# Performance work log

Measured on AMD Instinct MI355X. Metric: run time of the kernel, lower is better.

The kernel has to match this reference:

```python
import jax, jax.numpy as jnp
import numpy as np

B, N, K = 2, 16384, 8
NH, HD, CH, KV_IN = 4, 32, 128, 128
EPS = 1e-5

def layer_norm(x, g, b):
    mu = x.mean(-1, keepdims=True)
    var = ((x - mu) ** 2).mean(-1, keepdims=True)
    return (x - mu) / jnp.sqrt(var + EPS) * g + b

def setup_inputs() -> dict:
    key = jax.random.key(0)
    ks = jax.random.split(key, 8)
    s = 0.02
    return {
        "query_in": jax.random.normal(ks[0], (B, N, CH), jnp.float32),
        "kv_in": jax.random.normal(ks[1], (B, N, K, KV_IN), jnp.float32),
        "w_kv": jax.random.normal(ks[2], (KV_IN, 2 * NH * HD), jnp.float32) * s,
        "w_q": jax.random.normal(ks[3], (CH, NH * HD), jnp.float32) * s,
        "w_mh": jax.random.normal(ks[4], (NH * HD, CH), jnp.float32) * s,
        "b_mh": jnp.zeros((CH,), jnp.float32),
        "w1": jax.random.normal(ks[5], (CH, CH), jnp.float32) * s,
        "b1": jnp.zeros((CH,), jnp.float32),
        "w2": jax.random.normal(ks[6], (CH, CH), jnp.float32) * s,
        "b2": jnp.zeros((CH,), jnp.float32),
        "ln1_g": jnp.ones((CH,), jnp.float32),
        "ln1_b": jnp.zeros((CH,), jnp.float32),
        "ln2_g": jnp.ones((CH,), jnp.float32),
        "ln2_b": jnp.zeros((CH,), jnp.float32),
    }

def reference(query_in, kv_in, w_kv, w_q, w_mh, b_mh, w1, b1, w2, b2,
              ln1_g, ln1_b, ln2_g, ln2_b):
    # q projection: [B,N,CH] -> [B,N,NH,HD]
    q = (query_in @ w_q).reshape(B, N, NH, HD)
    # kv projection: [B,N,K,KV_IN] -> [B,N,K,2,NH,HD]; chunk(2) on last dim
    kv = (kv_in @ w_kv).reshape(B, N, K, 2, NH, HD)
    k, v = kv[..., 0, :, :], kv[..., 1, :, :]  # each [B,N,K,NH,HD]
    # per-token local attention over its own K keys
    sim = jnp.einsum('bnhd,bnkhd->bnhk', q, k) / np.sqrt(HD).astype(np.float32)
    attn = jax.nn.softmax(sim, axis=-1)
    out = jnp.einsum('bnhk,bnkhd->bnhd', attn, v).reshape(B, N, NH * HD)
    out = out @ w_mh + b_mh
    res = layer_norm(out, ln1_g, ln1_b) + query_in
    # GELU MLP (torch nn.GELU default = exact erf form)
    mlp = jax.nn.gelu(res @ w1 + b1, approximate=False) @ w2 + b2
    return layer_norm(mlp + res, ln2_g, ln2_b)
```

## Files before the change

### kernel.cpp

```cpp
#include <hip/hip_runtime.h>
#include <hip/hip_fp16.h>

typedef _Float16 f16x8 __attribute__((ext_vector_type(8)));
typedef float f32x4 __attribute__((ext_vector_type(4)));
typedef unsigned int uint32;

#define LDW 136
#define TB  16

#define WAITLGKM() do { __builtin_amdgcn_s_waitcnt(0xC07F); __builtin_amdgcn_sched_barrier(0); } while(0)

union F16x8U { f16x8 v; __half2 h2[4]; uint2 u2[2]; };

__device__ __forceinline__ uint32 pk2f(float a, float b) {
  __half2 h = __floats2half2_rn(a, b);
  return *reinterpret_cast<uint32*>(&h);
}
__device__ __forceinline__ float bcast(float v, int sl) {
  return __int_as_float(__builtin_amdgcn_readlane(__float_as_int(v), sl));
}
__device__ __forceinline__ float wred_sum(float v) {
  v += __shfl_xor(v, 32); v += __shfl_xor(v, 16); v += __shfl_xor(v, 8);
  v += __shfl_xor(v, 4);  v += __shfl_xor(v, 2);  v += __shfl_xor(v, 1);
  return v;
}
__device__ __forceinline__ f16x8 ldsv8(const __half* p) {
  return *reinterpret_cast<const f16x8*>(p);
}
__device__ __forceinline__ f32x4 mfma16(f16x8 a, f16x8 b, f32x4 c) {
  return __builtin_amdgcn_mfma_f32_16x16x32_f16(a, b, c, 0, 0, 0);
}
__device__ __forceinline__ void stp(__half* base, int fr, int fq, int nt, f32x4 a) {
  uint2 u; u.x = pk2f(a[0], a[1]); u.y = pk2f(a[2], a[3]);
  *reinterpret_cast<uint2*>(&base[fr * LDW + nt * 16 + fq * 4]) = u;
}

#define OFF_WQ   0
#define OFF_WK2  16384
#define OFF_WV   36864
#define OFF_WMH  53248
#define OFF_W1   69632
#define OFF_W2   86016
#define WS_HALVES 102400

__global__ void prep_weights(const float* __restrict__ wq, const float* __restrict__ wkv,
                             const float* __restrict__ wmh, const float* __restrict__ w1,
                             const float* __restrict__ w2, __half* __restrict__ ws) {
  int idx = blockIdx.x * 256 + threadIdx.x;
  if (idx >= WS_HALVES) return;
  float v;
  if (idx < OFF_WK2) {
    int t = idx, c = t >> 7, k = t & 127;
    v = wq[k * 128 + c];
  } else if (idx < OFF_WV) {
    int t = idx - OFF_WK2;
    int d = t % 40, row = t / 40;
    int h = row >> 7, i = row & 127;
    v = (d < 32) ? wkv[i * 256 + h * 32 + d] : 0.f;
  } else if (idx < OFF_WMH) {
    int t = idx - OFF_WV, c = t >> 7, k = t & 127;
    v = wkv[k * 256 + 128 + c];
  } else if (idx < OFF_W1) {
    int t = idx - OFF_WMH, c = t >> 7, k = t & 127;
    v = wmh[k * 128 + c];
  } else if (idx < OFF_W2) {
    int t = idx - OFF_W1, c = t >> 7, k = t & 127;
    v = w1[k * 128 + c];
  } else {
    int t = idx - OFF_W2, c = t >> 7, k = t & 127;
    v = w2[k * 128 + c];
  }
  ws[idx] = __float2half_rn(v);
}

#define LOADB2(GOFF, NT0, NT1, BF) do {                                          \
  _Pragma("unroll")                                                              \
  for (int t_ = 0; t_ < 2; ++t_) {                                               \
    int nt_ = t_ ? (NT1) : (NT0);                                                \
    _Pragma("unroll")                                                            \
    for (int ks_ = 0; ks_ < 4; ++ks_)                                            \
      BF[t_][ks_] = *reinterpret_cast<const f16x8*>(                             \
          wsv + (GOFF) + (nt_*16 + fr)*128 + ks_*32 + fq*8);                     \
  } } while (0)

#define GEMM2(AT, BF, ACC0, ACC1) do {                                           \
  _Pragma("unroll")                                                              \
  for (int ks_ = 0; ks_ < 4; ++ks_) {                                            \
    f16x8 b_ = ldsv8(&(AT)[fr * LDW + ks_ * 32 + fq * 8]);                       \
    ACC0 = mfma16(BF[0][ks_], b_, ACC0);                                         \
    ACC1 = mfma16(BF[1][ks_], b_, ACC1);                                         \
  } } while (0)

__global__ void __launch_bounds__(256, 6) ca_mfma(
    const float* __restrict__ xq, const float* __restrict__ kvin,
    const __half* __restrict__ wsv,
    const float* __restrict__ bmh, const float* __restrict__ b1,
    const float* __restrict__ b2,
    const float* __restrict__ g1, const float* __restrict__ bb1,
    const float* __restrict__ g2, const float* __restrict__ bb2,
    float* __restrict__ outp)
{
  __shared__ __half QWC[64 * LDW];
  __shared__ __half UBUF[2 * TB * LDW];

  const int tid = threadIdx.x;
  const int wv = tid >> 6, lane = tid & 63;
  const int fr = lane & 15, fq = lane >> 4;
  const int tb = blockIdx.x * TB;
  const int ltb = wv * 4;

  __half* Xh = UBUF;
  __half* Qb = UBUF + 2176;
  __half* Ob = UBUF;
  __half* Yb   = QWC;
  __half* RESb = QWC + 16 * LDW;
  __half* Hb   = QWC + 32 * LDW;
  __half* Vb   = QWC + 48 * LDW;

  const f32x4 ZZ = {0.f, 0.f, 0.f, 0.f};

  float4 pre[4];
  {
    const float4* kv4 = reinterpret_cast<const float4*>(kvin + (size_t)(tb + ltb) * 1024);
    pre[0] = kv4[2 * lane];       pre[1] = kv4[2 * lane + 1];
    pre[2] = kv4[2 * lane + 128]; pre[3] = kv4[2 * lane + 129];
  }
  f16x8 bf[2][4];
  LOADB2(OFF_WQ, wv, 4 + wv, bf);

  {
    int tok = tid >> 4, ko = (tid & 15) * 8;
    const float4* s0 = reinterpret_cast<const float4*>(xq + (size_t)(tb + tok) * 128 + ko);
    float4 a = s0[0], b = s0[1];
    uint4 u; u.x = pk2f(a.x, a.y); u.y = pk2f(a.z, a.w);
    u.z = pk2f(b.x, b.y); u.w = pk2f(b.z, b.w);
    *reinterpret_cast<uint4*>(&Xh[tok * LDW + ko]) = u;
  }
  __syncthreads();

  {
    f32x4 aA = ZZ, aB = ZZ;
    GEMM2(Xh, bf, aA, aB);
    stp(Qb, fr, fq, wv, aA);
    stp(Qb, fr, fq, 4 + wv, aB);
  }
  f16x8 bq[8];
#pragma unroll
  for (int nt = 0; nt < 8; ++nt)
    bq[nt] = *reinterpret_cast<const f16x8*>(
        wsv + OFF_WK2 + (wv * 128 + nt * 16 + fr) * 40 + fq * 8);
  __syncthreads();

  {
    f16x8 aq = ldsv8(&Qb[fr * LDW + wv * 32 + fq * 8]);
#pragma unroll
    for (int nt = 0; nt < 8; ++nt) {
      f32x4 acc = mfma16(bq[nt], aq, ZZ);
      uint2 u; u.x = pk2f(acc[0], acc[1]); u.y = pk2f(acc[2], acc[3]);
      *reinterpret_cast<uint2*>(&QWC[(wv * 16 + fr) * LDW + nt * 16 + fq * 4]) = u;
    }
  }
  __syncthreads();

  {
    const int p = lane & 31, hh = p >> 3, kk = p & 7, hf = lane >> 5;
    const int kr = lane >> 4, i8 = (lane & 15) * 8;
    const int l2 = 2 * lane;
    __half* kvw = UBUF + wv * 1088;
#pragma unroll 1
    for (int lt = 0; lt < 4; ++lt) {
      const int ltok = ltb + lt;
      WAITLGKM();
      {
        uint4 u0, u1;
        u0.x = pk2f(pre[0].x, pre[0].y); u0.y = pk2f(pre[0].z, pre[0].w);
        u0.z = pk2f(pre[1].x, pre[1].y); u0.w = pk2f(pre[1].z, pre[1].w);
        u1.x = pk2f(pre[2].x, pre[2].y); u1.y = pk2f(pre[2].z, pre[2].w);
        u1.z = pk2f(pre[3].x, pre[3].y); u1.w = pk2f(pre[3].z, pre[3].w);
        *reinterpret_cast<uint4*>(&kvw[kr * LDW + i8]) = u0;
        *reinterpret_cast<uint4*>(&kvw[(4 + kr) * LDW + i8]) = u1;
      }
      if (lt < 3) {
        const float4* kv4 = reinterpret_cast<const float4*>(kvin + (size_t)(tb + ltok + 1) * 1024);
        pre[0] = kv4[2 * lane];       pre[1] = kv4[2 * lane + 1];
        pre[2] = kv4[2 * lane + 128]; pre[3] = kv4[2 * lane + 129];
      }
      WAITLGKM();
      const __half* qrow = &QWC[(hh * 16 + ltok) * LDW + hf * 64];
      const __half* krow = &kvw[kk * LDW + hf * 64];
      __half2 s0 = __floats2half2_rn(0.f, 0.f), s1 = s0;
#pragma unroll
      for (int e = 0; e < 8; ++e) {
        F16x8U q8, k8;
        q8.v = ldsv8(qrow + e * 8);
        k8.v = ldsv8(krow + e * 8);
        s0 = __hfma2(q8.h2[0], k8.h2[0], s0);
        s1 = __hfma2(q8.h2[1], k8.h2[1], s1);
        s0 = __hfma2(q8.h2[2], k8.h2[2], s0);
        s1 = __hfma2(q8.h2[3], k8.h2[3], s1);
      }
      s0 = __hadd2(s0, s1);
      float acc = (__low2float(s0) + __high2float(s0)) * 0.17677669529663687f;
      acc += __shfl_xor(acc, 32);
      float m = acc;
      m = fmaxf(m, __shfl_xor(m, 1));
      m = fmaxf(m, __shfl_xor(m, 2));
      m = fmaxf(m, __shfl_xor(m, 4));
      float e = __expf(acc - m);
      float sden = e;
      sden += __shfl_xor(sden, 1); sden += __shfl_xor(sden, 2); sden += __shfl_xor(sden, 4);
      float at = __fdividef(e, sden);
      __half2 kvc[8];
#pragma unroll
      for (int k = 0; k < 8; ++k)
        kvc[k] = *reinterpret_cast<const __half2*>(&kvw[k * LDW + l2]);
#pragma unroll
      for (int h = 0; h < 4; ++h) {
        float c0 = 0.f, c1 = 0.f;
#pragma unroll
        for (int k = 0; k < 8; ++k) {
          float a = bcast(at, h * 8 + k);
          float2 kf = __half22float2(kvc[k]);
          c0 = fmaf(a, kf.x, c0);
          c1 = fmaf(a, kf.y, c1);
        }
        *reinterpret_cast<__half2*>(&QWC[(h * 16 + ltok) * LDW + l2]) =
            __floats2half2_rn(c0, c1);
      }
    }
  }
  LOADB2(OFF_WV, wv, 4 + wv, bf);
  __syncthreads();

  float2 xr[4];
#pragma unroll
  for (int lt = 0; lt < 4; ++lt) {
    int tok = tb + ltb + lt;
    xr[lt] = *reinterpret_cast<const float2*>(&xq[(size_t)tok * 128 + 2 * lane]);
  }
  {
    const int h1 = wv >> 1, h2 = 2 + (wv >> 1);
    f32x4 a1c = ZZ, a2c = ZZ;
#pragma unroll
    for (int ks = 0; ks < 4; ++ks) {
      f16x8 b1f = ldsv8(&QWC[(h1 * 16 + fr) * LDW + ks * 32 + fq * 8]);
      a1c = mfma16(bf[0][ks], b1f, a1c);
      f16x8 b2f = ldsv8(&QWC[(h2 * 16 + fr) * LDW + ks * 32 + fq * 8]);
      a2c = mfma16(bf[1][ks], b2f, a2c);
    }
    stp(Ob, fr, fq, wv, a1c);
    stp(Ob, fr, fq, 4 + wv, a2c);
  }
  LOADB2(OFF_WMH, wv, 4 + wv, bf);
  __syncthreads();

  {
    f32x4 aA = ZZ, aB = ZZ;
    GEMM2(Ob, bf, aA, aB);
    stp(Yb, fr, fq, wv, aA);
    stp(Yb, fr, fq, 4 + wv, aB);
  }
  LOADB2(OFF_W1, wv, 4 + wv, bf);
  __syncthreads();

  {
    const int l2 = 2 * lane;
    float2 bm = *reinterpret_cast<const float2*>(&bmh[l2]);
    float2 gg = *reinterpret_cast<const float2*>(&g1[l2]);
    float2 cc = *reinterpret_cast<const float2*>(&bb1[l2]);
#pragma unroll
    for (int lt = 0; lt < 4; ++lt) {
      int row = ltb + lt;
      float2 y = __half22float2(*reinterpret_cast<const __half2*>(&Yb[row * LDW + l2]));
      float v0 = y.x + bm.x, v1 = y.y + bm.y;
      float s = wred_sum(v0 + v1);
      float sq = wred_sum(v0 * v0 + v1 * v1);
      float mu = s * 0.0078125f;
      float var = sq * 0.0078125f - mu * mu;
      float rstd = rsqrtf(var + 1e-5f);
      float r0 = (v0 - mu) * rstd * gg.x + cc.x + xr[lt].x;
      float r1 = (v1 - mu) * rstd * gg.y + cc.y + xr[lt].y;
      *reinterpret_cast<__half2*>(&RESb[row * LDW + l2]) = __floats2half2_rn(r0, r1);
    }
  }
  __syncthreads();

  {
    f32x4 aA = ZZ, aB = ZZ;
    GEMM2(RESb, bf, aA, aB);
    int c0 = wv * 16 + fq * 4, c1 = 64 + wv * 16 + fq * 4;
    float4 b1a = *reinterpret_cast<const float4*>(&b1[c0]);
    float4 b1b = *reinterpret_cast<const float4*>(&b1[c1]);
    uint2 ua, ub;
    float t0, t1;
    t0 = aA[0] + b1a.x; t0 = 0.5f * t0 * (1.f + erff(t0 * 0.70710678118654752f));
    t1 = aA[1] + b1a.y; t1 = 0.5f * t1 * (1.f + erff(t1 * 0.70710678118654752f));
    ua.x = pk2f(t0, t1);
    t0 = aA[2] + b1a.z; t0 = 0.5f * t0 * (1.f + erff(t0 * 0.70710678118654752f));
    t1 = aA[3] + b1a.w; t1 = 0.5f * t1 * (1.f + erff(t1 * 0.70710678118654752f));
    ua.y = pk2f(t0, t1);
    t0 = aB[0] + b1b.x; t0 = 0.5f * t0 * (1.f + erff(t0 * 0.70710678118654752f));
    t1 = aB[1] + b1b.y; t1 = 0.5f * t1 * (1.f + erff(t1 * 0.70710678118654752f));
    ub.x = pk2f(t0, t1);
    t0 = aB[2] + b1b.z; t0 = 0.5f * t0 * (1.f + erff(t0 * 0.70710678118654752f));
    t1 = aB[3] + b1b.w; t1 = 0.5f * t1 * (1.f + erff(t1 * 0.70710678118654752f));
    ub.y = pk2f(t0, t1);
    *reinterpret_cast<uint2*>(&Hb[fr * LDW + c0]) = ua;
    *reinterpret_cast<uint2*>(&Hb[fr * LDW + c1]) = ub;
  }
  LOADB2(OFF_W2, wv, 4 + wv, bf);
  __syncthreads();

  {
    f32x4 aA = ZZ, aB = ZZ;
    GEMM2(Hb, bf, aA, aB);
    int c0 = wv * 16 + fq * 4, c1 = 64 + wv * 16 + fq * 4;
    float4 b2a = *reinterpret_cast<const float4*>(&b2[c0]);
    float4 b2b = *reinterpret_cast<const float4*>(&b2[c1]);
    F16x8U ra, rb;
    ra.u2[0] = *reinterpret_cast<const uint2*>(&RESb[fr * LDW + c0]);
    rb.u2[0] = *reinterpret_cast<const uint2*>(&RESb[fr * LDW + c1]);
    uint2 ua, ub;
    float2 p0 = __half22float2(ra.h2[0]), p1 = __half22float2(ra.h2[1]);
    ua.x = pk2f(aA[0] + b2a.x + p0.x, aA[1] + b2a.y + p0.y);
    ua.y = pk2f(aA[2] + b2a.z + p1.x, aA[3] + b2a.w + p1.y);
    float2 p2 = __half22float2(rb.h2[0]), p3 = __half22float2(rb.h2[1]);
    ub.x = pk2f(aB[0] + b2b.x + p2.x, aB[1] + b2b.y + p2.y);
    ub.y = pk2f(aB[2] + b2b.z + p3.x, aB[3] + b2b.w + p3.y);
    *reinterpret_cast<uint2*>(&Vb[fr * LDW + c0]) = ua;
    *reinterpret_cast<uint2*>(&Vb[fr * LDW + c1]) = ub;
  }
  __syncthreads();

  {
    const int l2 = 2 * lane;
    float2 gg = *reinterpret_cast<const float2*>(&g2[l2]);
    float2 cc = *reinterpret_cast<const float2*>(&bb2[l2]);
#pragma unroll
    for (int lt = 0; lt < 4; ++lt) {
      int row = ltb + lt, tok = tb + row;
      float2 v = __half22float2(*reinterpret_cast<const __half2*>(&Vb[row * LDW + l2]));
      float s = wred_sum(v.x + v.y);
      float sq = wred_sum(v.x * v.x + v.y * v.y);
      float mu = s * 0.0078125f;
      float var = sq * 0.0078125f - mu * mu;
      float rstd = rsqrtf(var + 1e-5f);
      float2 o;
      o.x = (v.x - mu) * rstd * gg.x + cc.x;
      o.y = (v.y - mu) * rstd * gg.y + cc.y;
      *reinterpret_cast<float2*>(&outp[(size_t)tok * 128 + l2]) = o;
    }
  }
}

extern "C" void kernel_launch(void* const* d_in, const int* in_sizes, int n_in,
                              void* d_out, int out_size, void* d_ws, size_t ws_size,
                              hipStream_t stream) {
  const float* xq = (const float*)d_in[0];
  const float* kv = (const float*)d_in[1];
  const float* wkv = (const float*)d_in[2];
  const float* wq = (const float*)d_in[3];
  const float* wmh = (const float*)d_in[4];
  const float* bmh = (const float*)d_in[5];
  const float* w1 = (const float*)d_in[6];
  const float* b1 = (const float*)d_in[7];
  const float* w2 = (const float*)d_in[8];
  const float* b2 = (const float*)d_in[9];
  const float* g1 = (const float*)d_in[10];
  const float* bb1 = (const float*)d_in[11];
  const float* g2 = (const float*)d_in[12];
  const float* bb2 = (const float*)d_in[13];
  __half* ws = (__half*)d_ws;

  prep_weights<<<(WS_HALVES + 255) / 256, 256, 0, stream>>>(wq, wkv, wmh, w1, w2, ws);

  const int tokens = 32768;
  ca_mfma<<<tokens / TB, 256, 0, stream>>>(xq, kv, ws, bmh, b1, b2,
                                           g1, bb1, g2, bb2, (float*)d_out);
}
```

Before: 65.62 us.

## Double token tile to 32 with 512-thread blocks and shuffle-based Q transpose

Doubles the tokens per block to 32 and the block size to 512 threads (8 waves split into two 16-token halves). Each wave's weight fragments now cover more tokens, and there are fewer blocks in total. The Q projection result is rearranged into the MFMA operand layout with cross-lane shuffles instead of a round trip through LDS, which removes one barrier. The trade-offs are a larger LDS footprint per block and a 512-thread launch bound that may lower occupancy.

```diff
diff --git a/kernel.cpp b/kernel.cpp
--- a/kernel.cpp
+++ b/kernel.cpp
@@ -6,11 +6,11 @@
 typedef unsigned int uint32;
 
 #define LDW 136
-#define TB  16
+#define TB  32
 
 #define WAITLGKM() do { __builtin_amdgcn_s_waitcnt(0xC07F); __builtin_amdgcn_sched_barrier(0); } while(0)
 
-union F16x8U { f16x8 v; __half2 h2[4]; uint2 u2[2]; };
+union F16x8U { f16x8 v; __half2 h2[4]; uint2 u2[2]; uint4 u4; };
 
 __device__ __forceinline__ uint32 pk2f(float a, float b) {
   __half2 h = __floats2half2_rn(a, b);
@@ -91,7 +91,7 @@
     ACC1 = mfma16(BF[1][ks_], b_, ACC1);                                         \
   } } while (0)
 
-__global__ void __launch_bounds__(256, 6) ca_mfma(
+__global__ void __launch_bounds__(512, 6) ca_mfma(
     const float* __restrict__ xq, const float* __restrict__ kvin,
     const __half* __restrict__ wsv,
     const float* __restrict__ bmh, const float* __restrict__ b1,
@@ -100,22 +100,22 @@
     const float* __restrict__ g2, const float* __restrict__ bb2,
     float* __restrict__ outp)
 {
-  __shared__ __half QWC[64 * LDW];
-  __shared__ __half UBUF[2 * TB * LDW];
+  __shared__ __half QWC[128 * LDW];
+  __shared__ __half UBUF[8 * 1088];
 
   const int tid = threadIdx.x;
   const int wv = tid >> 6, lane = tid & 63;
+  const int wl = wv & 3, tt = wv >> 2;
   const int fr = lane & 15, fq = lane >> 4;
   const int tb = blockIdx.x * TB;
   const int ltb = wv * 4;
 
   __half* Xh = UBUF;
-  __half* Qb = UBUF + 2176;
   __half* Ob = UBUF;
   __half* Yb   = QWC;
-  __half* RESb = QWC + 16 * LDW;
-  __half* Hb   = QWC + 32 * LDW;
-  __half* Vb   = QWC + 48 * LDW;
+  __half* RESb = QWC + 32 * LDW;
+  __half* Hb   = QWC + 64 * LDW;
+  __half* Vb   = QWC + 96 * LDW;
 
   const f32x4 ZZ = {0.f, 0.f, 0.f, 0.f};
 
@@ -126,7 +126,7 @@
     pre[2] = kv4[2 * lane + 128]; pre[3] = kv4[2 * lane + 129];
   }
   f16x8 bf[2][4];
-  LOADB2(OFF_WQ, wv, 4 + wv, bf);
+  LOADB2(OFF_WQ, 2 * wl, 2 * wl + 1, bf);
 
   {
     int tok = tid >> 4, ko = (tid & 15) * 8;
@@ -138,26 +138,37 @@
   }
   __syncthreads();
 
+  f16x8 aq;
   {
     f32x4 aA = ZZ, aB = ZZ;
-    GEMM2(Xh, bf, aA, aB);
-    stp(Qb, fr, fq, wv, aA);
-    stp(Qb, fr, fq, 4 + wv, aB);
-  }
-  f16x8 bq[8];
-#pragma unroll
-  for (int nt = 0; nt < 8; ++nt)
-    bq[nt] = *reinterpret_cast<const f16x8*>(
-        wsv + OFF_WK2 + (wv * 128 + nt * 16 + fr) * 40 + fq * 8);
-  __syncthreads();
-
-  {
-    f16x8 aq = ldsv8(&Qb[fr * LDW + wv * 32 + fq * 8]);
+    GEMM2(Xh + tt * 16 * LDW, bf, aA, aB);
+    uint32 w0a = pk2f(aA[0], aA[1]), w1a = pk2f(aA[2], aA[3]);
+    uint32 w0b = pk2f(aB[0], aB[1]), w1b = pk2f(aB[2], aB[3]);
+    int srcA = fr + 32 * (fq & 1), srcB = srcA + 16;
+    uint32 a0A = (uint32)__shfl((int)w0a, srcA), a1A = (uint32)__shfl((int)w1a, srcA);
+    uint32 b0A = (uint32)__shfl((int)w0b, srcA), b1A = (uint32)__shfl((int)w1b, srcA);
+    uint32 a0B = (uint32)__shfl((int)w0a, srcB), a1B = (uint32)__shfl((int)w1a, srcB);
+    uint32 b0B = (uint32)__shfl((int)w0b, srcB), b1B = (uint32)__shfl((int)w1b, srcB);
+    bool thi = (fq >> 1) != 0;
+    F16x8U bu;
+    bu.u4.x = thi ? b0A : a0A;
+    bu.u4.y = thi ? b1A : a1A;
+    bu.u4.z = thi ? b0B : a0B;
+    bu.u4.w = thi ? b1B : a1B;
+    aq = bu.v;
+  }
+
+  {
+    f16x8 bq[8];
+#pragma unroll
+    for (int nt = 0; nt < 8; ++nt)
+      bq[nt] = *reinterpret_cast<const f16x8*>(
+          wsv + OFF_WK2 + (wl * 128 + nt * 16 + fr) * 40 + fq * 8);
 #pragma unroll
     for (int nt = 0; nt < 8; ++nt) {
       f32x4 acc = mfma16(bq[nt], aq, ZZ);
       uint2 u; u.x = pk2f(acc[0], acc[1]); u.y = pk2f(acc[2], acc[3]);
-      *reinterpret_cast<uint2*>(&QWC[(wv * 16 + fr) * LDW + nt * 16 + fq * 4]) = u;
+      *reinterpret_cast<uint2*>(&QWC[(wl * 32 + tt * 16 + fr) * LDW + nt * 16 + fq * 4]) = u;
     }
   }
   __syncthreads();
@@ -169,7 +180,7 @@
     __half* kvw = UBUF + wv * 1088;
 #pragma unroll 1
     for (int lt = 0; lt < 4; ++lt) {
-      const int ltok = ltb + lt;
+      const int gtok = ltb + lt;
       WAITLGKM();
       {
         uint4 u0, u1;
@@ -181,12 +192,12 @@
         *reinterpret_cast<uint4*>(&kvw[(4 + kr) * LDW + i8]) = u1;
       }
       if (lt < 3) {
-        const float4* kv4 = reinterpret_cast<const float4*>(kvin + (size_t)(tb + ltok + 1) * 1024);
+        const float4* kv4 = reinterpret_cast<const float4*>(kvin + (size_t)(tb + gtok + 1) * 1024);
         pre[0] = kv4[2 * lane];       pre[1] = kv4[2 * lane + 1];
         pre[2] = kv4[2 * lane + 128]; pre[3] = kv4[2 * lane + 129];
       }
       WAITLGKM();
-      const __half* qrow = &QWC[(hh * 16 + ltok) * LDW + hf * 64];
+      const __half* qrow = &QWC[(hh * 32 + gtok) * LDW + hf * 64];
       const __half* krow = &kvw[kk * LDW + hf * 64];
       __half2 s0 = __floats2half2_rn(0.f, 0.f), s1 = s0;
 #pragma unroll
@@ -224,12 +235,12 @@
           c0 = fmaf(a, kf.x, c0);
           c1 = fmaf(a, kf.y, c1);
         }
-        *reinterpret_cast<__half2*>(&QWC[(h * 16 + ltok) * LDW + l2]) =
+        *reinterpret_cast<__half2*>(&QWC[(h * 32 + gtok) * LDW + l2]) =
             __floats2half2_rn(c0, c1);
       }
     }
   }
-  LOADB2(OFF_WV, wv, 4 + wv, bf);
+  LOADB2(OFF_WV, wl, 4 + wl, bf);
   __syncthreads();
 
   float2 xr[4];
@@ -239,28 +250,28 @@
     xr[lt] = *reinterpret_cast<const float2*>(&xq[(size_t)tok * 128 + 2 * lane]);
   }
   {
-    const int h1 = wv >> 1, h2 = 2 + (wv >> 1);
+    const int h1 = wl >> 1, h2 = 2 + (wl >> 1);
     f32x4 a1c = ZZ, a2c = ZZ;
 #pragma unroll
     for (int ks = 0; ks < 4; ++ks) {
-      f16x8 b1f = ldsv8(&QWC[(h1 * 16 + fr) * LDW + ks * 32 + fq * 8]);
+      f16x8 b1f = ldsv8(&QWC[(h1 * 32 + tt * 16 + fr) * LDW + ks * 32 + fq * 8]);
       a1c = mfma16(bf[0][ks], b1f, a1c);
-      f16x8 b2f = ldsv8(&QWC[(h2 * 16 + fr) * LDW + ks * 32 + fq * 8]);
+      f16x8 b2f = ldsv8(&QWC[(h2 * 32 + tt * 16 + fr) * LDW + ks * 32 + fq * 8]);
       a2c = mfma16(bf[1][ks], b2f, a2c);
     }
-    stp(Ob, fr, fq, wv, a1c);
-    stp(Ob, fr, fq, 4 + wv, a2c);
-  }
-  LOADB2(OFF_WMH, wv, 4 + wv, bf);
+    stp(Ob + tt * 16 * LDW, fr, fq, wl, a1c);
+    stp(Ob + tt * 16 * LDW, fr, fq, 4 + wl, a2c);
+  }
+  LOADB2(OFF_WMH, wl, 4 + wl, bf);
   __syncthreads();
 
   {
     f32x4 aA = ZZ, aB = ZZ;
-    GEMM2(Ob, bf, aA, aB);
-    stp(Yb, fr, fq, wv, aA);
-    stp(Yb, fr, fq, 4 + wv, aB);
-  }
-  LOADB2(OFF_W1, wv, 4 + wv, bf);
+    GEMM2(Ob + tt * 16 * LDW, bf, aA, aB);
+    stp(Yb + tt * 16 * LDW, fr, fq, wl, aA);
+    stp(Yb + tt * 16 * LDW, fr, fq, 4 + wl, aB);
+  }
+  LOADB2(OFF_W1, wl, 4 + wl, bf);
   __syncthreads();
 
   {
@@ -287,8 +298,8 @@
 
   {
     f32x4 aA = ZZ, aB = ZZ;
-    GEMM2(RESb, bf, aA, aB);
-    int c0 = wv * 16 + fq * 4, c1 = 64 + wv * 16 + fq * 4;
+    GEMM2(RESb + tt * 16 * LDW, bf, aA, aB);
+    int c0 = wl * 16 + fq * 4, c1 = 64 + wl * 16 + fq * 4;
     float4 b1a = *reinterpret_cast<const float4*>(&b1[c0]);
     float4 b1b = *reinterpret_cast<const float4*>(&b1[c1]);
     uint2 ua, ub;
@@ -305,21 +316,21 @@
     t0 = aB[2] + b1b.z; t0 = 0.5f * t0 * (1.f + erff(t0 * 0.70710678118654752f));
     t1 = aB[3] + b1b.w; t1 = 0.5f * t1 * (1.f + erff(t1 * 0.70710678118654752f));
     ub.y = pk2f(t0, t1);
-    *reinterpret_cast<uint2*>(&Hb[fr * LDW + c0]) = ua;
-    *reinterpret_cast<uint2*>(&Hb[fr * LDW + c1]) = ub;
-  }
-  LOADB2(OFF_W2, wv, 4 + wv, bf);
+    *reinterpret_cast<uint2*>(&Hb[(tt * 16 + fr) * LDW + c0]) = ua;
+    *reinterpret_cast<uint2*>(&Hb[(tt * 16 + fr) * LDW + c1]) = ub;
+  }
+  LOADB2(OFF_W2, wl, 4 + wl, bf);
   __syncthreads();
 
   {
     f32x4 aA = ZZ, aB = ZZ;
-    GEMM2(Hb, bf, aA, aB);
-    int c0 = wv * 16 + fq * 4, c1 = 64 + wv * 16 + fq * 4;
+    GEMM2(Hb + tt * 16 * LDW, bf, aA, aB);
+    int c0 = wl * 16 + fq * 4, c1 = 64 + wl * 16 + fq * 4;
     float4 b2a = *reinterpret_cast<const float4*>(&b2[c0]);
     float4 b2b = *reinterpret_cast<const float4*>(&b2[c1]);
     F16x8U ra, rb;
-    ra.u2[0] = *reinterpret_cast<const uint2*>(&RESb[fr * LDW + c0]);
-    rb.u2[0] = *reinterpret_cast<const uint2*>(&RESb[fr * LDW + c1]);
+    ra.u2[0] = *reinterpret_cast<const uint2*>(&RESb[(tt * 16 + fr) * LDW + c0]);
+    rb.u2[0] = *reinterpret_cast<const uint2*>(&RESb[(tt * 16 + fr) * LDW + c1]);
     uint2 ua, ub;
     float2 p0 = __half22float2(ra.h2[0]), p1 = __half22float2(ra.h2[1]);
     ua.x = pk2f(aA[0] + b2a.x + p0.x, aA[1] + b2a.y + p0.y);
@@ -327,8 +338,8 @@
     float2 p2 = __half22float2(rb.h2[0]), p3 = __half22float2(rb.h2[1]);
     ub.x = pk2f(aB[0] + b2b.x + p2.x, aB[1] + b2b.y + p2.y);
     ub.y = pk2f(aB[2] + b2b.z + p3.x, aB[3] + b2b.w + p3.y);
-    *reinterpret_cast<uint2*>(&Vb[fr * LDW + c0]) = ua;
-    *reinterpret_cast<uint2*>(&Vb[fr * LDW + c1]) = ub;
+    *reinterpret_cast<uint2*>(&Vb[(tt * 16 + fr) * LDW + c0]) = ua;
+    *reinterpret_cast<uint2*>(&Vb[(tt * 16 + fr) * LDW + c1]) = ub;
   }
   __syncthreads();
 
@@ -375,6 +386,6 @@
   prep_weights<<<(WS_HALVES + 255) / 256, 256, 0, stream>>>(wq, wkv, wmh, w1, w2, ws);
 
   const int tokens = 32768;
-  ca_mfma<<<tokens / TB, 256, 0, stream>>>(xq, kv, ws, bmh, b1, b2,
+  ca_mfma<<<tokens / TB, 512, 0, stream>>>(xq, kv, ws, bmh, b1, b2,
                                            g1, bb1, g2, bb2, (float*)d_out);
 }
```

After: 75.55 us. 15.1% more time.
